# Kernel tuning notes

Measured on AMD Instinct MI355X. Metric: run time of the kernel, lower is better.

The kernel has to match this reference:

```python
import jax, jax.numpy as jnp
import numpy as np

B, CIN, COUT, N, T, K = 16, 32, 64, 1024, 64, 3


def setup_inputs() -> dict:
    key = jax.random.key(0)
    k1, k2, k3 = jax.random.split(key, 3)
    x = jax.random.normal(k1, (B, CIN, N, T), dtype=jnp.float32)
    # scaled laplacian-like support (keep spectral radius ~1 so Chebyshev terms stay bounded)
    adj = jax.random.normal(k2, (N, N), dtype=jnp.float32) / np.sqrt(N).astype(np.float32)
    W = jax.random.normal(k3, (4 * COUT, (CIN + COUT) * K), dtype=jnp.float32) * 0.02
    b = jnp.zeros((4 * COUT,), dtype=jnp.float32)
    return {"x": x, "adj": adj, "W": W, "b": b}


def reference(x, adj, W, b):
    Bn, cin, Nn, Tn = x.shape
    c_out = W.shape[0] // 4
    feat_in = W.shape[1] // K  # = cin + c_out

    # Chebyshev polynomial basis of adj (loop-invariant across time; compute once)
    Ls = [jnp.eye(Nn, dtype=x.dtype), adj]
    for _ in range(2, K):
        Ls.append(2.0 * (adj @ Ls[-1]) - Ls[-2])
    Lap = jnp.stack(Ls, 0)  # [K, N, N]; Ls[k][q, n]

    # Conv1d(kernel=1) weight reshaped to match channel flatten order (c major, k minor)
    Wr = W.reshape(4 * c_out, feat_in, K)  # [4*c_out, F, K]
    bb = b[None, :, None]

    def step(carry, xt):
        h, c = carry
        tem = jnp.concatenate([xt, h], axis=1)  # [B, F, N]
        # einsum('bcn,knq->bckq', x, Lap.T) == einsum('bfn,kqn->bfkq', x, Lap)
        g = jnp.einsum('bfn,kqn->bfkq', tem, Lap)  # [B, F, K, N]
        fea = jnp.einsum('bfkq,ofk->boq', g, Wr) + bb  # [B, 4*c_out, N]
        i, j, f, o = jnp.split(fea, 4, axis=1)
        new_c = c * jax.nn.sigmoid(f) + jax.nn.sigmoid(i) * jnp.tanh(j)
        new_h = jnp.tanh(new_c) * jax.nn.sigmoid(o)
        return (new_h, new_c), new_h

    h0 = jnp.zeros((Bn, c_out, Nn), dtype=x.dtype)
    c0 = jnp.zeros((Bn, c_out, Nn), dtype=x.dtype)
    x_t = jnp.moveaxis(x, -1, 0)  # [T, B, cin, N]
    _, outs = jax.lax.scan(step, (h0, c0), x_t)  # [T, B, c_out, N]
    return jnp.moveaxis(outs, 0, -1)  # [B, c_out, N, T]
```

## Files before the change

kernel.cpp:

```cpp
#include <hip/hip_runtime.h>
#include <stdint.h>


#define Bb   16
#define CIN  32
#define COUT 64
#define Nn   1024
#define Tt   64
#define Ff   96
#define G4   256
#define KJ   288

#define BUFSZ 40960
#define GQPB  624
#define GQLO  19968

typedef unsigned short u16;
typedef short short8 __attribute__((ext_vector_type(8)));
typedef short short4v __attribute__((ext_vector_type(4)));
typedef float f32x4 __attribute__((ext_vector_type(4)));

static __device__ __forceinline__ u16 f2bf(float f) {
    union { float f; uint32_t u; } v; v.f = f;
    uint32_t r = v.u + 0x7FFFu + ((v.u >> 16) & 1u);
    return (u16)(r >> 16);
}
static __device__ __forceinline__ float bf2f(u16 h) {
    union { uint32_t u; float f; } v; v.u = ((uint32_t)h) << 16;
    return v.f;
}
static __device__ __forceinline__ float sigm(float x) { return 1.0f / (1.0f + expf(-x)); }

static __device__ __forceinline__ void gload16(const void* g, void* l) {
    __builtin_amdgcn_global_load_lds(
        (const __attribute__((address_space(1))) void*)g,
        (__attribute__((address_space(3))) void*)l, 16, 0, 0);
}

__global__ void k_fill(float* out, int n, float v) {
    int i = blockIdx.x * 256 + threadIdx.x;
    if (i < n) out[i] = v;
}

__global__ __launch_bounds__(256) void k_adj_split(const float* __restrict__ adj,
                                                   u16* __restrict__ hi, u16* __restrict__ lo) {
    int i = blockIdx.x * 256 + threadIdx.x;
    float v = adj[i];
    u16 h = f2bf(v);
    hi[i] = h; lo[i] = f2bf(v - bf2f(h));
}

__global__ __launch_bounds__(256) void k_adj_t(const float* __restrict__ adj,
                                               u16* __restrict__ th, u16* __restrict__ tl_) {
    __shared__ float tile[64][65];
    int m0 = blockIdx.x * 64, n0 = blockIdx.y * 64;
    int tid = threadIdx.x;
    #pragma unroll
    for (int i = 0; i < 16; i++) {
        int lin = i * 256 + tid;
        int ml = lin >> 6, nl = lin & 63;
        tile[ml][nl] = adj[(size_t)(m0 + ml) * Nn + n0 + nl];
    }
    __syncthreads();
    #pragma unroll
    for (int i = 0; i < 16; i++) {
        int lin = i * 256 + tid;
        int nl = lin >> 6, ml = lin & 63;
        float v = tile[ml][nl];
        u16 h = f2bf(v);
        size_t off = (size_t)(n0 + nl) * Nn + m0 + ml;
        th[off] = h; tl_[off] = f2bf(v - bf2f(h));
    }
}

__global__ __launch_bounds__(256) void k_l2(
    const u16* __restrict__ a_hi, const u16* __restrict__ a_lo,
    const u16* __restrict__ bt_hi, const u16* __restrict__ bt_lo,
    u16* __restrict__ o_hi, u16* __restrict__ o_lo)
{
    __shared__ u16 Ah[64][40], Al[64][40], Bh[64][40], Bl[64][40];
    const int tid = threadIdx.x, lane = tid & 63, w = tid >> 6;
    const int wm = (w >> 1) * 32, wn = (w & 1) * 32;
    const int r0 = blockIdx.x * 64, q0 = blockIdx.y * 64;
    const int srow = tid >> 2, scol = (tid & 3) * 8;
    const u16* arh = a_hi + (size_t)(r0 + srow) * Nn;
    const u16* arl = a_lo + (size_t)(r0 + srow) * Nn;
    const u16* brh = bt_hi + (size_t)(q0 + srow) * Nn;
    const u16* brl = bt_lo + (size_t)(q0 + srow) * Nn;

    f32x4 acc[2][2];
    #pragma unroll
    for (int i = 0; i < 2; i++)
        #pragma unroll
        for (int j = 0; j < 2; j++) acc[i][j] = (f32x4){0.f, 0.f, 0.f, 0.f};

    for (int k0 = 0; k0 < Nn; k0 += 32) {
        __syncthreads();
        *(short8*)&Ah[srow][scol] = *(const short8*)&arh[k0 + scol];
        *(short8*)&Al[srow][scol] = *(const short8*)&arl[k0 + scol];
        *(short8*)&Bh[srow][scol] = *(const short8*)&brh[k0 + scol];
        *(short8*)&Bl[srow][scol] = *(const short8*)&brl[k0 + scol];
        __syncthreads();
        const int kb = (lane >> 4) * 8;
        short8 ah[2], al[2], bh[2], bl[2];
        #pragma unroll
        for (int mi = 0; mi < 2; mi++) {
            int row = wm + mi * 16 + (lane & 15);
            ah[mi] = *(const short8*)&Ah[row][kb];
            al[mi] = *(const short8*)&Al[row][kb];
        }
        #pragma unroll
        for (int ni = 0; ni < 2; ni++) {
            int col = wn + ni * 16 + (lane & 15);
            bh[ni] = *(const short8*)&Bh[col][kb];
            bl[ni] = *(const short8*)&Bl[col][kb];
        }
        #pragma unroll
        for (int mi = 0; mi < 2; mi++)
            #pragma unroll
            for (int ni = 0; ni < 2; ni++) {
                acc[mi][ni] = __builtin_amdgcn_mfma_f32_16x16x32_bf16(ah[mi], bh[ni], acc[mi][ni], 0, 0, 0);
                acc[mi][ni] = __builtin_amdgcn_mfma_f32_16x16x32_bf16(al[mi], bh[ni], acc[mi][ni], 0, 0, 0);
                acc[mi][ni] = __builtin_amdgcn_mfma_f32_16x16x32_bf16(ah[mi], bl[ni], acc[mi][ni], 0, 0, 0);
            }
    }
    #pragma unroll
    for (int mi = 0; mi < 2; mi++)
        #pragma unroll
        for (int ni = 0; ni < 2; ni++)
            #pragma unroll
            for (int j = 0; j < 4; j++) {
                int rr = r0 + wm + mi * 16 + (lane >> 4) * 4 + j;
                int qq = q0 + wn + ni * 16 + (lane & 15);
                float v = 2.f * acc[mi][ni][j] - ((rr == qq) ? 1.f : 0.f);
                size_t off = (size_t)rr * Nn + qq;
                u16 hh = f2bf(v);
                o_hi[off] = hh; o_lo[off] = f2bf(v - bf2f(hh));
            }
}

__global__ __launch_bounds__(256) void k_w_split(const float* __restrict__ W,
                                                 u16* __restrict__ hi, u16* __restrict__ lo) {
    int idx = blockIdx.x * 256 + threadIdx.x;
    int o = idx / KJ, j = idx - o * KJ;
    int k = j / Ff, f = j - k * Ff;
    float v = W[(size_t)o * KJ + f * 3 + k];
    u16 h = f2bf(v);
    hi[idx] = h; lo[idx] = f2bf(v - bf2f(h));
}

__global__ __launch_bounds__(256) void k_x_split(const float* __restrict__ x,
        u16* __restrict__ xf_hi, u16* __restrict__ xf_lo) {
    __shared__ float tile[64][65];
    int n0 = blockIdx.x * 64;
    int bc = blockIdx.y;
    const float* src = x + (size_t)bc * Nn * Tt;
    int tid = threadIdx.x;
    #pragma unroll
    for (int i = 0; i < 16; i++) {
        int lin = i * 256 + tid;
        int nl = lin >> 6, tl = lin & 63;
        tile[nl][tl] = src[(size_t)(n0 + nl) * Tt + tl];
    }
    __syncthreads();
    int b = bc >> 5, ch = bc & 31;
    #pragma unroll
    for (int i = 0; i < 16; i++) {
        int lin = i * 256 + tid;
        int tl = lin >> 6, nl = lin & 63;
        float v = tile[nl][tl];
        u16 h = f2bf(v), l = f2bf(v - bf2f(h));
        size_t off = (((size_t)tl * Bb + b) * CIN + ch) * Nn + n0 + nl;
        xf_hi[off] = h; xf_lo[off] = l;
    }
}

__global__ __launch_bounds__(512, 4) void k_step(
    int t,
    const u16* __restrict__ xsf_hi, const u16* __restrict__ xsf_lo,
    u16* __restrict__ hf_hi, u16* __restrict__ hf_lo,
    const u16* __restrict__ bcat_hi, const u16* __restrict__ bcat_lo,
    const u16* __restrict__ Wh, const u16* __restrict__ Wl,
    const float* __restrict__ bias, float* __restrict__ cbuf,
    float* __restrict__ outbuf)
{
    __shared__ __attribute__((aligned(16))) char lds[81920];
    const int tid = threadIdx.x, lane = tid & 63, w = tid >> 6;
    const int bx = blockIdx.x;
    const int q0g = bx * 32;
    const int bb = blockIdx.y;

    const u16* srcb[5];
    #pragma unroll
    for (int i = 0; i < 5; i++) {
        int u = i * 512 + tid;
        if (u < 1536) {
            int hl = (u >= 768) ? 1 : 0;
            int r = (u - hl * 768) >> 3, c8 = u & 7;
            const u16* p;
            if (r < CIN) p = (hl ? xsf_lo : xsf_hi) + (size_t)((t * Bb + bb) * CIN + r) * Nn;
            else         p = (hl ? hf_lo  : hf_hi ) + (size_t)(bb * COUT + r - CIN) * Nn;
            srcb[i] = p + (c8 ^ (r & 7)) * 8;
        } else {
            int v = u - 1536;
            int hl = v >> 9;
            int r = (v & 511) >> 3, c8 = v & 7;
            int grow = q0g + (r & 31) + ((r >= 32) ? Nn : 0);
            srcb[i] = (hl ? bcat_lo : bcat_hi) + (size_t)grow * Nn + (c8 ^ (r & 7)) * 8;
        }
    }

    const int wr = w >> 2, wc = w & 3;
    f32x4 acc[3];
    #pragma unroll
    for (int i = 0; i < 3; i++) acc[i] = (f32x4){0.f, 0.f, 0.f, 0.f};

    u16 cxh[6], cxl[6];
    #pragma unroll
    for (int i = 0; i < 6; i++) { cxh[i] = 0; cxl[i] = 0; }
    const int capkc = bx >> 1;

    #pragma unroll
    for (int i = 0; i < 5; i++)
        gload16(srcb[i], lds + (i * 512 + tid) * 16);

    for (int kc = 0; kc < 16; kc++) {
        if (kc < 15) {
            char* nb = lds + ((kc + 1) & 1) * BUFSZ;
            const int k0 = (kc + 1) * 64;
            #pragma unroll
            for (int i = 0; i < 5; i++)
                gload16(srcb[i] + k0, nb + (i * 512 + tid) * 16);
            asm volatile("s_waitcnt vmcnt(5)" ::: "memory");
        } else {
            asm volatile("s_waitcnt vmcnt(0)" ::: "memory");
        }
        __builtin_amdgcn_s_barrier();
        const char* bo = lds + (kc & 1) * BUFSZ;
        #pragma unroll
        for (int kk = 0; kk < 2; kk++) {
            const int ksw = kk * 4 + (lane >> 4);
            short8 ah[3], al[3], bh, bl;
            #pragma unroll
            for (int mi = 0; mi < 3; mi++) {
                int r = wr * 48 + mi * 16 + (lane & 15);
                int off = r * 128 + ((ksw ^ (r & 7)) << 4);
                ah[mi] = *(const short8*)(bo + off);
                al[mi] = *(const short8*)(bo + 12288 + off);
            }
            {
                int rb = wc * 16 + (lane & 15);
                int off = 24576 + rb * 128 + ((ksw ^ (rb & 7)) << 4);
                bh = *(const short8*)(bo + off);
                bl = *(const short8*)(bo + 8192 + off);
            }
            #pragma unroll
            for (int mi = 0; mi < 3; mi++) {
                acc[mi] = __builtin_amdgcn_mfma_f32_16x16x32_bf16(ah[mi], bh, acc[mi], 0, 0, 0);
                acc[mi] = __builtin_amdgcn_mfma_f32_16x16x32_bf16(al[mi], bh, acc[mi], 0, 0, 0);
                acc[mi] = __builtin_amdgcn_mfma_f32_16x16x32_bf16(ah[mi], bl, acc[mi], 0, 0, 0);
            }
        }
        if (kc == capkc) {
            int q = lane & 31;
            int jg = (w << 1) | (lane >> 5);
            int lc = ((bx & 1) << 5) | q;
            int u8 = lc >> 3, byoff = (lc & 7) * 2;
            #pragma unroll
            for (int jj = 0; jj < 6; jj++) {
                int j = jg * 6 + jj;
                int off = j * 128 + (((u8) ^ (j & 7)) << 4) + byoff;
                cxh[jj] = *(const u16*)(bo + off);
                cxl[jj] = *(const u16*)(bo + 12288 + off);
            }
            asm volatile("s_waitcnt lgkmcnt(0)" ::: "memory");
            __builtin_amdgcn_sched_barrier(0);
        }
        __builtin_amdgcn_s_barrier();
    }

    {
        int q = lane & 31;
        int jg = (w << 1) | (lane >> 5);
        #pragma unroll
        for (int jj = 0; jj < 6; jj++) {
            int j = jg * 6 + jj;
            *(u16*)(lds + q * GQPB + j * 2) = cxh[jj];
            *(u16*)(lds + GQLO + q * GQPB + j * 2) = cxl[jj];
        }
    }
    #pragma unroll
    for (int mi = 0; mi < 3; mi++) {
        int c = wc * 16 + (lane & 15);
        int g = c >> 5, ql = c & 31;
        int f0 = wr * 48 + mi * 16 + (lane >> 4) * 4;
        int jd = 96 + g * 96 + f0;
        short4v vh, vl;
        #pragma unroll
        for (int j = 0; j < 4; j++) {
            float v = acc[mi][j];
            u16 hh = f2bf(v);
            vh[j] = (short)hh;
            vl[j] = (short)f2bf(v - bf2f(hh));
        }
        *(short4v*)(lds + ql * GQPB + jd * 2) = vh;
        *(short4v*)(lds + GQLO + ql * GQPB + jd * 2) = vl;
    }
    __syncthreads();

    f32x4 a2[2][2];
    #pragma unroll
    for (int i = 0; i < 2; i++)
        #pragma unroll
        for (int j = 0; j < 2; j++) a2[i][j] = (f32x4){0.f, 0.f, 0.f, 0.f};

    const int kb8 = (lane >> 4) * 8;
    #pragma unroll
    for (int c = 0; c < 9; c++) {
        int j0 = c * 32;
        short8 wh[2], wl2[2], gh[2], gl[2];
        #pragma unroll
        for (int mi = 0; mi < 2; mi++) {
            int o = w * 32 + mi * 16 + (lane & 15);
            size_t so = (size_t)o * KJ + j0 + kb8;
            wh[mi]  = *(const short8*)&Wh[so];
            wl2[mi] = *(const short8*)&Wl[so];
        }
        #pragma unroll
        for (int ni = 0; ni < 2; ni++) {
            int q = ni * 16 + (lane & 15);
            int off = q * GQPB + (j0 + kb8) * 2;
            gh[ni] = *(const short8*)(lds + off);
            gl[ni] = *(const short8*)(lds + GQLO + off);
        }
        #pragma unroll
        for (int mi = 0; mi < 2; mi++)
            #pragma unroll
            for (int ni = 0; ni < 2; ni++) {
                a2[mi][ni] = __builtin_amdgcn_mfma_f32_16x16x32_bf16(wh[mi],  gh[ni], a2[mi][ni], 0, 0, 0);
                a2[mi][ni] = __builtin_amdgcn_mfma_f32_16x16x32_bf16(wl2[mi], gh[ni], a2[mi][ni], 0, 0, 0);
                a2[mi][ni] = __builtin_amdgcn_mfma_f32_16x16x32_bf16(wh[mi],  gl[ni], a2[mi][ni], 0, 0, 0);
            }
    }
    __syncthreads();

    {
        float* FEAf = (float*)lds;
        #pragma unroll
        for (int mi = 0; mi < 2; mi++) {
            int o0 = w * 32 + mi * 16 + (lane >> 4) * 4;
            f32x4 bv = *(const f32x4*)&bias[o0];
            #pragma unroll
            for (int ni = 0; ni < 2; ni++) {
                int q = ni * 16 + (lane & 15);
                #pragma unroll
                for (int j = 0; j < 4; j++)
                    FEAf[(o0 + j) * 33 + q] = a2[mi][ni][j] + bv[j];
            }
        }
    }
    __syncthreads();

    {
        const float* FEAf = (const float*)lds;
        int q = tid & 31, qg = q0g + q;
        int co0 = (tid >> 5) * 4;
        #pragma unroll
        for (int ii = 0; ii < 4; ii++) {
            int co = co0 + ii;
            float iv = FEAf[co * 33 + q];
            float jv = FEAf[(co + 64) * 33 + q];
            float fv = FEAf[(co + 128) * 33 + q];
            float ov = FEAf[(co + 192) * 33 + q];
            size_t cof = ((size_t)(bb * COUT + co)) * Nn + qg;
            float cc = cbuf[cof];
            float nc = cc * sigm(fv) + sigm(iv) * tanhf(jv);
            float nh = tanhf(nc) * sigm(ov);
            cbuf[cof] = nc;
            u16 hh = f2bf(nh);
            hf_hi[cof] = hh; hf_lo[cof] = f2bf(nh - bf2f(hh));
            outbuf[((size_t)(t * Bb + bb) * COUT + co) * Nn + qg] = nh;
        }
    }
}

__global__ __launch_bounds__(256) void k_out_t(const float* __restrict__ outbuf,
                                               float* __restrict__ out) {
    __shared__ float tile[64][65];
    int q0 = blockIdx.x * 64;
    int bo = blockIdx.y;
    int b = bo >> 6, o = bo & 63;
    int tid = threadIdx.x;
    #pragma unroll
    for (int i = 0; i < 16; i++) {
        int lin = i * 256 + tid;
        int tl = lin >> 6, ql = lin & 63;
        tile[tl][ql] = outbuf[(((size_t)tl * Bb + b) * COUT + o) * Nn + q0 + ql];
    }
    __syncthreads();
    #pragma unroll
    for (int i = 0; i < 16; i++) {
        int lin = i * 256 + tid;
        int ql = lin >> 6, tl = lin & 63;
        out[((size_t)bo * Nn + q0 + ql) * Tt + tl] = tile[tl][ql];
    }
}

extern "C" void kernel_launch(void* const* d_in, const int* in_sizes, int n_in,
                              void* d_out, int out_size, void* d_ws, size_t ws_size,
                              hipStream_t stream)
{
    const float* x    = (const float*)d_in[0];
    const float* adj  = (const float*)d_in[1];
    const float* W    = (const float*)d_in[2];
    const float* bias = (const float*)d_in[3];
    float* out = (float*)d_out;

    size_t off = 0;
    char* base = (char*)d_ws;
    auto take = [&](size_t bytes) -> void* {
        void* r = base + off;
        off += (bytes + 255) & ~(size_t)255;
        return r;
    };
    u16* bcat_hi = (u16*)take(2ull * 2 * Nn * Nn);
    u16* bcat_lo = (u16*)take(2ull * 2 * Nn * Nn);
    u16* adjT_hi = (u16*)take(2ull * Nn * Nn);
    u16* adjT_lo = (u16*)take(2ull * Nn * Nn);
    u16* xsf_hi  = (u16*)take(2ull * Tt * Bb * CIN * Nn);
    u16* xsf_lo  = (u16*)take(2ull * Tt * Bb * CIN * Nn);
    u16* hf_hi   = (u16*)take(2ull * Bb * COUT * Nn);
    u16* hf_lo   = (u16*)take(2ull * Bb * COUT * Nn);
    float* cbuf  = (float*)take(4ull * Bb * COUT * Nn);
    u16* Wc_hi   = (u16*)take(2ull * G4 * KJ);
    u16* Wc_lo   = (u16*)take(2ull * G4 * KJ);
    float* outbuf = (float*)take(4ull * (size_t)Tt * Bb * COUT * Nn);

    if (off > ws_size) {
        float v = (float)(ws_size >> 20);
        k_fill<<<dim3((out_size + 255) / 256), 256, 0, stream>>>(out, out_size, v);
        return;
    }

    hipMemsetAsync(hf_hi, 0, 2ull * Bb * COUT * Nn, stream);
    hipMemsetAsync(hf_lo, 0, 2ull * Bb * COUT * Nn, stream);
    hipMemsetAsync(cbuf, 0, 4ull * Bb * COUT * Nn, stream);

    k_adj_split<<<dim3((Nn * Nn) / 256), 256, 0, stream>>>(adj, bcat_hi, bcat_lo);
    k_adj_t<<<dim3(16, 16), 256, 0, stream>>>(adj, adjT_hi, adjT_lo);
    k_l2<<<dim3(16, 16), 256, 0, stream>>>(bcat_hi, bcat_lo, adjT_hi, adjT_lo,
                                           bcat_hi + (size_t)Nn * Nn, bcat_lo + (size_t)Nn * Nn);
    k_w_split<<<dim3((G4 * KJ) / 256), 256, 0, stream>>>(W, Wc_hi, Wc_lo);
    k_x_split<<<dim3(Nn / 64, Bb * CIN), 256, 0, stream>>>(x, xsf_hi, xsf_lo);

    for (int t = 0; t < Tt; t++) {
        k_step<<<dim3(32, 16), 512, 0, stream>>>(t,
            xsf_hi, xsf_lo, hf_hi, hf_lo,
            bcat_hi, bcat_lo, Wc_hi, Wc_lo,
            bias, cbuf, outbuf);
    }
    k_out_t<<<dim3(Nn / 64, Bb * COUT), 256, 0, stream>>>(outbuf, out);
}
```

Baseline: 2.565 ms.

## Double k_step tile to 64 nodes with 1024-thread blocks and swizzled grid

```diff
diff --git a/kernel.cpp b/kernel.cpp
--- a/kernel.cpp
+++ b/kernel.cpp
@@ -11,9 +11,12 @@
 #define G4   256
 #define KJ   288
 
-#define BUFSZ 40960
+#define BUFSZ 65536
+#define AOLO  12288
+#define BOHI  24576
+#define BOLO  40960
 #define GQPB  624
-#define GQLO  19968
+#define GQLO  39936
 
 typedef unsigned short u16;
 typedef short short8 __attribute__((ext_vector_type(8)));
@@ -165,17 +168,24 @@
     __syncthreads();
     int b = bc >> 5, ch = bc & 31;
     #pragma unroll
-    for (int i = 0; i < 16; i++) {
-        int lin = i * 256 + tid;
-        int tl = lin >> 6, nl = lin & 63;
-        float v = tile[nl][tl];
-        u16 h = f2bf(v), l = f2bf(v - bf2f(h));
-        size_t off = (((size_t)tl * Bb + b) * CIN + ch) * Nn + n0 + nl;
-        xf_hi[off] = h; xf_lo[off] = l;
-    }
-}
-
-__global__ __launch_bounds__(512, 4) void k_step(
+    for (int i = 0; i < 2; i++) {
+        int item = i * 256 + tid;
+        int tl = item >> 3, oct = item & 7;
+        short8 vh, vl;
+        #pragma unroll
+        for (int m = 0; m < 8; m++) {
+            float v = tile[oct * 8 + m][tl];
+            u16 h = f2bf(v);
+            vh[m] = (short)h;
+            vl[m] = (short)f2bf(v - bf2f(h));
+        }
+        size_t off = (((size_t)tl * Bb + b) * CIN + ch) * Nn + n0 + oct * 8;
+        *(short8*)&xf_hi[off] = vh;
+        *(short8*)&xf_lo[off] = vl;
+    }
+}
+
+__global__ __launch_bounds__(1024, 4) void k_step(
     int t,
     const u16* __restrict__ xsf_hi, const u16* __restrict__ xsf_lo,
     u16* __restrict__ hf_hi, u16* __restrict__ hf_lo,
@@ -184,16 +194,18 @@
     const float* __restrict__ bias, float* __restrict__ cbuf,
     float* __restrict__ outbuf)
 {
-    __shared__ __attribute__((aligned(16))) char lds[81920];
+    __shared__ __attribute__((aligned(16))) char lds[131072];
     const int tid = threadIdx.x, lane = tid & 63, w = tid >> 6;
-    const int bx = blockIdx.x;
-    const int q0g = bx * 32;
-    const int bb = blockIdx.y;
-
-    const u16* srcb[5];
-    #pragma unroll
-    for (int i = 0; i < 5; i++) {
-        int u = i * 512 + tid;
+    const int bid = blockIdx.x;
+    const int swz = (bid & 7) * 32 + (bid >> 3);
+    const int qt = swz >> 4;
+    const int bb = swz & 15;
+    const int q0g = qt * 64;
+
+    const u16* srcb[4];
+    #pragma unroll
+    for (int i = 0; i < 4; i++) {
+        int u = i * 1024 + tid;
         if (u < 1536) {
             int hl = (u >= 768) ? 1 : 0;
             int r = (u - hl * 768) >> 3, c8 = u & 7;
@@ -201,16 +213,18 @@
             if (r < CIN) p = (hl ? xsf_lo : xsf_hi) + (size_t)((t * Bb + bb) * CIN + r) * Nn;
             else         p = (hl ? hf_lo  : hf_hi ) + (size_t)(bb * COUT + r - CIN) * Nn;
             srcb[i] = p + (c8 ^ (r & 7)) * 8;
+        } else if (u < 3584) {
+            int v = u - 1536;
+            int hl = v >> 10;
+            int r = (v & 1023) >> 3, c8 = v & 7;
+            int grow = q0g + (r & 63) + ((r >= 64) ? Nn : 0);
+            srcb[i] = (hl ? bcat_lo : bcat_hi) + (size_t)grow * Nn + (c8 ^ (r & 7)) * 8;
         } else {
-            int v = u - 1536;
-            int hl = v >> 9;
-            int r = (v & 511) >> 3, c8 = v & 7;
-            int grow = q0g + (r & 31) + ((r >= 32) ? Nn : 0);
-            srcb[i] = (hl ? bcat_lo : bcat_hi) + (size_t)grow * Nn + (c8 ^ (r & 7)) * 8;
-        }
-    }
-
-    const int wr = w >> 2, wc = w & 3;
+            srcb[i] = bcat_hi + (u & 1023) * 8;
+        }
+    }
+
+    const int wr = w >> 3, wc = w & 7;
     f32x4 acc[3];
     #pragma unroll
     for (int i = 0; i < 3; i++) acc[i] = (f32x4){0.f, 0.f, 0.f, 0.f};
@@ -218,20 +232,19 @@
     u16 cxh[6], cxl[6];
     #pragma unroll
     for (int i = 0; i < 6; i++) { cxh[i] = 0; cxl[i] = 0; }
-    const int capkc = bx >> 1;
-
-    #pragma unroll
-    for (int i = 0; i < 5; i++)
-        gload16(srcb[i], lds + (i * 512 + tid) * 16);
+
+    #pragma unroll
+    for (int i = 0; i < 4; i++)
+        gload16(srcb[i], lds + (i * 1024 + tid) * 16);
 
     for (int kc = 0; kc < 16; kc++) {
         if (kc < 15) {
             char* nb = lds + ((kc + 1) & 1) * BUFSZ;
             const int k0 = (kc + 1) * 64;
             #pragma unroll
-            for (int i = 0; i < 5; i++)
-                gload16(srcb[i] + k0, nb + (i * 512 + tid) * 16);
-            asm volatile("s_waitcnt vmcnt(5)" ::: "memory");
+            for (int i = 0; i < 4; i++)
+                gload16(srcb[i] + k0, nb + (i * 1024 + tid) * 16);
+            asm volatile("s_waitcnt vmcnt(4)" ::: "memory");
         } else {
             asm volatile("s_waitcnt vmcnt(0)" ::: "memory");
         }
@@ -246,13 +259,13 @@
                 int r = wr * 48 + mi * 16 + (lane & 15);
                 int off = r * 128 + ((ksw ^ (r & 7)) << 4);
                 ah[mi] = *(const short8*)(bo + off);
-                al[mi] = *(const short8*)(bo + 12288 + off);
+                al[mi] = *(const short8*)(bo + AOLO + off);
             }
             {
                 int rb = wc * 16 + (lane & 15);
-                int off = 24576 + rb * 128 + ((ksw ^ (rb & 7)) << 4);
-                bh = *(const short8*)(bo + off);
-                bl = *(const short8*)(bo + 8192 + off);
+                int off = rb * 128 + ((ksw ^ (rb & 7)) << 4);
+                bh = *(const short8*)(bo + BOHI + off);
+                bl = *(const short8*)(bo + BOLO + off);
             }
             #pragma unroll
             for (int mi = 0; mi < 3; mi++) {
@@ -261,17 +274,13 @@
                 acc[mi] = __builtin_amdgcn_mfma_f32_16x16x32_bf16(ah[mi], bl, acc[mi], 0, 0, 0);
             }
         }
-        if (kc == capkc) {
-            int q = lane & 31;
-            int jg = (w << 1) | (lane >> 5);
-            int lc = ((bx & 1) << 5) | q;
-            int u8 = lc >> 3, byoff = (lc & 7) * 2;
+        if (kc == qt) {
             #pragma unroll
             for (int jj = 0; jj < 6; jj++) {
-                int j = jg * 6 + jj;
-                int off = j * 128 + (((u8) ^ (j & 7)) << 4) + byoff;
+                int j = w * 6 + jj;
+                int off = j * 128 + ((((lane >> 3)) ^ (j & 7)) << 4) + (lane & 7) * 2;
                 cxh[jj] = *(const u16*)(bo + off);
-                cxl[jj] = *(const u16*)(bo + 12288 + off);
+                cxl[jj] = *(const u16*)(bo + AOLO + off);
             }
             asm volatile("s_waitcnt lgkmcnt(0)" ::: "memory");
             __builtin_amdgcn_sched_barrier(0);
@@ -280,19 +289,17 @@
     }
 
     {
-        int q = lane & 31;
-        int jg = (w << 1) | (lane >> 5);
         #pragma unroll
         for (int jj = 0; jj < 6; jj++) {
-            int j = jg * 6 + jj;
-            *(u16*)(lds + q * GQPB + j * 2) = cxh[jj];
-            *(u16*)(lds + GQLO + q * GQPB + j * 2) = cxl[jj];
+            int j = w * 6 + jj;
+            *(u16*)(lds + lane * GQPB + j * 2) = cxh[jj];
+            *(u16*)(lds + GQLO + lane * GQPB + j * 2) = cxl[jj];
         }
     }
     #pragma unroll
     for (int mi = 0; mi < 3; mi++) {
         int c = wc * 16 + (lane & 15);
-        int g = c >> 5, ql = c & 31;
+        int g = c >> 6, ql = c & 63;
         int f0 = wr * 48 + mi * 16 + (lane >> 4) * 4;
         int jd = 96 + g * 96 + f0;
         short4v vh, vl;
@@ -314,6 +321,7 @@
         #pragma unroll
         for (int j = 0; j < 2; j++) a2[i][j] = (f32x4){0.f, 0.f, 0.f, 0.f};
 
+    const int wo = w >> 1, wq = w & 1;
     const int kb8 = (lane >> 4) * 8;
     #pragma unroll
     for (int c = 0; c < 9; c++) {
@@ -321,14 +329,14 @@
         short8 wh[2], wl2[2], gh[2], gl[2];
         #pragma unroll
         for (int mi = 0; mi < 2; mi++) {
-            int o = w * 32 + mi * 16 + (lane & 15);
+            int o = wo * 32 + mi * 16 + (lane & 15);
             size_t so = (size_t)o * KJ + j0 + kb8;
             wh[mi]  = *(const short8*)&Wh[so];
             wl2[mi] = *(const short8*)&Wl[so];
         }
         #pragma unroll
         for (int ni = 0; ni < 2; ni++) {
-            int q = ni * 16 + (lane & 15);
+            int q = wq * 32 + ni * 16 + (lane & 15);
             int off = q * GQPB + (j0 + kb8) * 2;
             gh[ni] = *(const short8*)(lds + off);
             gl[ni] = *(const short8*)(lds + GQLO + off);
@@ -348,14 +356,14 @@
         float* FEAf = (float*)lds;
         #pragma unroll
         for (int mi = 0; mi < 2; mi++) {
-            int o0 = w * 32 + mi * 16 + (lane >> 4) * 4;
+            int o0 = wo * 32 + mi * 16 + (lane >> 4) * 4;
             f32x4 bv = *(const f32x4*)&bias[o0];
             #pragma unroll
             for (int ni = 0; ni < 2; ni++) {
-                int q = ni * 16 + (lane & 15);
+                int q = wq * 32 + ni * 16 + (lane & 15);
                 #pragma unroll
                 for (int j = 0; j < 4; j++)
-                    FEAf[(o0 + j) * 33 + q] = a2[mi][ni][j] + bv[j];
+                    FEAf[(o0 + j) * 65 + q] = a2[mi][ni][j] + bv[j];
             }
         }
     }
@@ -363,15 +371,15 @@
 
     {
         const float* FEAf = (const float*)lds;
-        int q = tid & 31, qg = q0g + q;
-        int co0 = (tid >> 5) * 4;
+        int q = tid & 63, qg = q0g + q;
+        int co0 = (tid >> 6) * 4;
         #pragma unroll
         for (int ii = 0; ii < 4; ii++) {
             int co = co0 + ii;
-            float iv = FEAf[co * 33 + q];
-            float jv = FEAf[(co + 64) * 33 + q];
-            float fv = FEAf[(co + 128) * 33 + q];
-            float ov = FEAf[(co + 192) * 33 + q];
+            float iv = FEAf[co * 65 + q];
+            float jv = FEAf[(co + 64) * 65 + q];
+            float fv = FEAf[(co + 128) * 65 + q];
+            float ov = FEAf[(co + 192) * 65 + q];
             size_t cof = ((size_t)(bb * COUT + co)) * Nn + qg;
             float cc = cbuf[cof];
             float nc = cc * sigm(fv) + sigm(iv) * tanhf(jv);
@@ -454,7 +462,7 @@
     k_x_split<<<dim3(Nn / 64, Bb * CIN), 256, 0, stream>>>(x, xsf_hi, xsf_lo);
 
     for (int t = 0; t < Tt; t++) {
-        k_step<<<dim3(32, 16), 512, 0, stream>>>(t,
+        k_step<<<dim3(256), 1024, 0, stream>>>(t,
             xsf_hi, xsf_lo, hf_hi, hf_lo,
             bcat_hi, bcat_lo, Wc_hi, Wc_lo,
             bias, cbuf, outbuf);
```

New measurement: 2.783 ms. 8.5% more time.

## Split graph GEMM K across wave groups, widen per-wave tile, vectorize x split stores

Applied to the files above, without the earlier changes.

```diff
diff --git a/kernel.cpp b/kernel.cpp
--- a/kernel.cpp
+++ b/kernel.cpp
@@ -14,6 +14,7 @@
 #define BUFSZ 40960
 #define GQPB  624
 #define GQLO  19968
+#define SCP   100
 
 typedef unsigned short u16;
 typedef short short8 __attribute__((ext_vector_type(8)));
@@ -165,13 +166,20 @@
     __syncthreads();
     int b = bc >> 5, ch = bc & 31;
     #pragma unroll
-    for (int i = 0; i < 16; i++) {
-        int lin = i * 256 + tid;
-        int tl = lin >> 6, nl = lin & 63;
-        float v = tile[nl][tl];
-        u16 h = f2bf(v), l = f2bf(v - bf2f(h));
-        size_t off = (((size_t)tl * Bb + b) * CIN + ch) * Nn + n0 + nl;
-        xf_hi[off] = h; xf_lo[off] = l;
+    for (int i = 0; i < 2; i++) {
+        int item = i * 256 + tid;
+        int tl = item >> 3, oct = item & 7;
+        short8 vh, vl;
+        #pragma unroll
+        for (int m = 0; m < 8; m++) {
+            float v = tile[oct * 8 + m][tl];
+            u16 h = f2bf(v);
+            vh[m] = (short)h;
+            vl[m] = (short)f2bf(v - bf2f(h));
+        }
+        size_t off = (((size_t)tl * Bb + b) * CIN + ch) * Nn + n0 + oct * 8;
+        *(short8*)&xf_hi[off] = vh;
+        *(short8*)&xf_lo[off] = vl;
     }
 }
 
@@ -210,10 +218,16 @@
         }
     }
 
-    const int wr = w >> 2, wc = w & 3;
-    f32x4 acc[3];
-    #pragma unroll
-    for (int i = 0; i < 3; i++) acc[i] = (f32x4){0.f, 0.f, 0.f, 0.f};
+    const int kg = w >> 2;
+    const int wsub = w & 3;
+    const int wr = wsub >> 1, wc = wsub & 1;
+    const int ksw = kg * 4 + (lane >> 4);
+
+    f32x4 acc[3][2];
+    #pragma unroll
+    for (int i = 0; i < 3; i++)
+        #pragma unroll
+        for (int j = 0; j < 2; j++) acc[i][j] = (f32x4){0.f, 0.f, 0.f, 0.f};
 
     u16 cxh[6], cxl[6];
     #pragma unroll
@@ -237,10 +251,8 @@
         }
         __builtin_amdgcn_s_barrier();
         const char* bo = lds + (kc & 1) * BUFSZ;
-        #pragma unroll
-        for (int kk = 0; kk < 2; kk++) {
-            const int ksw = kk * 4 + (lane >> 4);
-            short8 ah[3], al[3], bh, bl;
+        {
+            short8 ah[3], al[3], bh[2], bl[2];
             #pragma unroll
             for (int mi = 0; mi < 3; mi++) {
                 int r = wr * 48 + mi * 16 + (lane & 15);
@@ -248,18 +260,23 @@
                 ah[mi] = *(const short8*)(bo + off);
                 al[mi] = *(const short8*)(bo + 12288 + off);
             }
-            {
-                int rb = wc * 16 + (lane & 15);
+            #pragma unroll
+            for (int ni = 0; ni < 2; ni++) {
+                int rb = wc * 32 + ni * 16 + (lane & 15);
                 int off = 24576 + rb * 128 + ((ksw ^ (rb & 7)) << 4);
-                bh = *(const short8*)(bo + off);
-                bl = *(const short8*)(bo + 8192 + off);
-            }
-            #pragma unroll
-            for (int mi = 0; mi < 3; mi++) {
-                acc[mi] = __builtin_amdgcn_mfma_f32_16x16x32_bf16(ah[mi], bh, acc[mi], 0, 0, 0);
-                acc[mi] = __builtin_amdgcn_mfma_f32_16x16x32_bf16(al[mi], bh, acc[mi], 0, 0, 0);
-                acc[mi] = __builtin_amdgcn_mfma_f32_16x16x32_bf16(ah[mi], bl, acc[mi], 0, 0, 0);
-            }
+                bh[ni] = *(const short8*)(bo + off);
+                bl[ni] = *(const short8*)(bo + 8192 + off);
+            }
+            __builtin_amdgcn_s_setprio(1);
+            #pragma unroll
+            for (int mi = 0; mi < 3; mi++)
+                #pragma unroll
+                for (int ni = 0; ni < 2; ni++) {
+                    acc[mi][ni] = __builtin_amdgcn_mfma_f32_16x16x32_bf16(ah[mi], bh[ni], acc[mi][ni], 0, 0, 0);
+                    acc[mi][ni] = __builtin_amdgcn_mfma_f32_16x16x32_bf16(al[mi], bh[ni], acc[mi][ni], 0, 0, 0);
+                    acc[mi][ni] = __builtin_amdgcn_mfma_f32_16x16x32_bf16(ah[mi], bl[ni], acc[mi][ni], 0, 0, 0);
+                }
+            __builtin_amdgcn_s_setprio(0);
         }
         if (kc == capkc) {
             int q = lane & 31;
@@ -280,6 +297,31 @@
     }
 
     {
+        float* scratch = (float*)(lds + BUFSZ);
+        if (kg == 0) {
+            #pragma unroll
+            for (int mi = 0; mi < 3; mi++)
+                #pragma unroll
+                for (int ni = 0; ni < 2; ni++) {
+                    int c = wc * 32 + ni * 16 + (lane & 15);
+                    int r0 = wr * 48 + mi * 16 + (lane >> 4) * 4;
+                    *(f32x4*)&scratch[c * SCP + r0] = acc[mi][ni];
+                }
+        }
+        __syncthreads();
+        if (kg == 1) {
+            #pragma unroll
+            for (int mi = 0; mi < 3; mi++)
+                #pragma unroll
+                for (int ni = 0; ni < 2; ni++) {
+                    int c = wc * 32 + ni * 16 + (lane & 15);
+                    int r0 = wr * 48 + mi * 16 + (lane >> 4) * 4;
+                    acc[mi][ni] += *(const f32x4*)&scratch[c * SCP + r0];
+                }
+        }
+    }
+
+    {
         int q = lane & 31;
         int jg = (w << 1) | (lane >> 5);
         #pragma unroll
@@ -289,22 +331,26 @@
             *(u16*)(lds + GQLO + q * GQPB + j * 2) = cxl[jj];
         }
     }
-    #pragma unroll
-    for (int mi = 0; mi < 3; mi++) {
-        int c = wc * 16 + (lane & 15);
-        int g = c >> 5, ql = c & 31;
-        int f0 = wr * 48 + mi * 16 + (lane >> 4) * 4;
-        int jd = 96 + g * 96 + f0;
-        short4v vh, vl;
-        #pragma unroll
-        for (int j = 0; j < 4; j++) {
-            float v = acc[mi][j];
-            u16 hh = f2bf(v);
-            vh[j] = (short)hh;
-            vl[j] = (short)f2bf(v - bf2f(hh));
-        }
-        *(short4v*)(lds + ql * GQPB + jd * 2) = vh;
-        *(short4v*)(lds + GQLO + ql * GQPB + jd * 2) = vl;
+    if (kg == 1) {
+        #pragma unroll
+        for (int mi = 0; mi < 3; mi++)
+            #pragma unroll
+            for (int ni = 0; ni < 2; ni++) {
+                int c = wc * 32 + ni * 16 + (lane & 15);
+                int g = c >> 5, ql = c & 31;
+                int f0 = wr * 48 + mi * 16 + (lane >> 4) * 4;
+                int jd = 96 + g * 96 + f0;
+                short4v vh, vl;
+                #pragma unroll
+                for (int j = 0; j < 4; j++) {
+                    float v = acc[mi][ni][j];
+                    u16 hh = f2bf(v);
+                    vh[j] = (short)hh;
+                    vl[j] = (short)f2bf(v - bf2f(hh));
+                }
+                *(short4v*)(lds + ql * GQPB + jd * 2) = vh;
+                *(short4v*)(lds + GQLO + ql * GQPB + jd * 2) = vl;
+            }
     }
     __syncthreads();
 
```

Result: faster. 2.514 ms (-2.0%).

## Halve k-chunk size, shrink LDS, ping-pong hidden state, vectorize x split

Applied to the files above, without the earlier changes.

```diff
diff --git a/kernel.cpp b/kernel.cpp
--- a/kernel.cpp
+++ b/kernel.cpp
@@ -11,9 +11,14 @@
 #define G4   256
 #define KJ   288
 
-#define BUFSZ 40960
+#define BUFSZ 20480
+#define AHI   0
+#define ALO   6144
+#define BHI   12288
+#define BLO   16384
 #define GQPB  624
 #define GQLO  19968
+#define NCHUNK 32
 
 typedef unsigned short u16;
 typedef short short8 __attribute__((ext_vector_type(8)));
@@ -165,52 +170,68 @@
     __syncthreads();
     int b = bc >> 5, ch = bc & 31;
     #pragma unroll
-    for (int i = 0; i < 16; i++) {
-        int lin = i * 256 + tid;
-        int tl = lin >> 6, nl = lin & 63;
-        float v = tile[nl][tl];
-        u16 h = f2bf(v), l = f2bf(v - bf2f(h));
-        size_t off = (((size_t)tl * Bb + b) * CIN + ch) * Nn + n0 + nl;
-        xf_hi[off] = h; xf_lo[off] = l;
-    }
-}
-
-__global__ __launch_bounds__(512, 4) void k_step(
+    for (int i = 0; i < 2; i++) {
+        int item = i * 256 + tid;
+        int tl = item >> 3, oct = item & 7;
+        short8 vh, vl;
+        #pragma unroll
+        for (int m = 0; m < 8; m++) {
+            float v = tile[oct * 8 + m][tl];
+            u16 h = f2bf(v);
+            vh[m] = (short)h;
+            vl[m] = (short)f2bf(v - bf2f(h));
+        }
+        size_t off = (((size_t)tl * Bb + b) * CIN + ch) * Nn + n0 + oct * 8;
+        *(short8*)&xf_hi[off] = vh;
+        *(short8*)&xf_lo[off] = vl;
+    }
+}
+
+__global__ __launch_bounds__(512, 8) void k_step(
     int t,
     const u16* __restrict__ xsf_hi, const u16* __restrict__ xsf_lo,
-    u16* __restrict__ hf_hi, u16* __restrict__ hf_lo,
+    const u16* __restrict__ hin_hi, const u16* __restrict__ hin_lo,
+    u16* __restrict__ hout_hi, u16* __restrict__ hout_lo,
     const u16* __restrict__ bcat_hi, const u16* __restrict__ bcat_lo,
     const u16* __restrict__ Wh, const u16* __restrict__ Wl,
     const float* __restrict__ bias, float* __restrict__ cbuf,
     float* __restrict__ outbuf)
 {
-    __shared__ __attribute__((aligned(16))) char lds[81920];
+    __shared__ __attribute__((aligned(16))) char lds[40960];
     const int tid = threadIdx.x, lane = tid & 63, w = tid >> 6;
     const int bx = blockIdx.x;
     const int q0g = bx * 32;
     const int bb = blockIdx.y;
 
-    const u16* srcb[5];
-    #pragma unroll
-    for (int i = 0; i < 5; i++) {
-        int u = i * 512 + tid;
-        if (u < 1536) {
-            int hl = (u >= 768) ? 1 : 0;
-            int r = (u - hl * 768) >> 3, c8 = u & 7;
+    const u16* srcb[3];
+    #pragma unroll
+    for (int i = 0; i < 3; i++) {
+        int u = i * 512 + ((i == 2) ? (tid & 255) : tid);
+        if (u < 768) {
+            int hl = (u >= 384) ? 1 : 0;
+            int ua = u - hl * 384;
+            int R = ua >> 3, sp = ua & 7;
+            int s = sp ^ (R & 7);
+            int r = 2 * R + (s >> 2), c4 = s & 3;
             const u16* p;
             if (r < CIN) p = (hl ? xsf_lo : xsf_hi) + (size_t)((t * Bb + bb) * CIN + r) * Nn;
-            else         p = (hl ? hf_lo  : hf_hi ) + (size_t)(bb * COUT + r - CIN) * Nn;
-            srcb[i] = p + (c8 ^ (r & 7)) * 8;
+            else         p = (hl ? hin_lo : hin_hi) + (size_t)(bb * COUT + r - CIN) * Nn;
+            srcb[i] = p + c4 * 8;
         } else {
-            int v = u - 1536;
-            int hl = v >> 9;
-            int r = (v & 511) >> 3, c8 = v & 7;
-            int grow = q0g + (r & 31) + ((r >= 32) ? Nn : 0);
-            srcb[i] = (hl ? bcat_lo : bcat_hi) + (size_t)grow * Nn + (c8 ^ (r & 7)) * 8;
+            int hl = (u >= 1024) ? 1 : 0;
+            int ub = u - 768 - hl * 256;
+            int R = ub >> 3, sp = ub & 7;
+            int s = sp ^ (R & 7);
+            int rloc = 2 * R + (s >> 2), c4 = s & 3;
+            int grow = q0g + (rloc & 31) + ((rloc >= 32) ? Nn : 0);
+            srcb[i] = (hl ? bcat_lo : bcat_hi) + (size_t)grow * Nn + c4 * 8;
         }
     }
 
     const int wr = w >> 2, wc = w & 3;
+    const int ksw = lane >> 4;
+    const int capkc = bx;
+
     f32x4 acc[3];
     #pragma unroll
     for (int i = 0; i < 3; i++) acc[i] = (f32x4){0.f, 0.f, 0.f, 0.f};
@@ -218,60 +239,64 @@
     u16 cxh[6], cxl[6];
     #pragma unroll
     for (int i = 0; i < 6; i++) { cxh[i] = 0; cxl[i] = 0; }
-    const int capkc = bx >> 1;
-
-    #pragma unroll
-    for (int i = 0; i < 5; i++)
-        gload16(srcb[i], lds + (i * 512 + tid) * 16);
-
-    for (int kc = 0; kc < 16; kc++) {
-        if (kc < 15) {
+
+    gload16(srcb[0], lds + (size_t)tid * 16);
+    gload16(srcb[1], lds + (size_t)(512 + tid) * 16);
+    if (tid < 256) gload16(srcb[2], lds + (size_t)(1024 + tid) * 16);
+
+    for (int kc = 0; kc < NCHUNK; kc++) {
+        if (kc < NCHUNK - 1) {
             char* nb = lds + ((kc + 1) & 1) * BUFSZ;
-            const int k0 = (kc + 1) * 64;
-            #pragma unroll
-            for (int i = 0; i < 5; i++)
-                gload16(srcb[i] + k0, nb + (i * 512 + tid) * 16);
-            asm volatile("s_waitcnt vmcnt(5)" ::: "memory");
+            const int k0 = (kc + 1) * 32;
+            gload16(srcb[0] + k0, nb + (size_t)tid * 16);
+            gload16(srcb[1] + k0, nb + (size_t)(512 + tid) * 16);
+            if (tid < 256) gload16(srcb[2] + k0, nb + (size_t)(1024 + tid) * 16);
+            if (w < 4) { asm volatile("s_waitcnt vmcnt(3)" ::: "memory"); }
+            else       { asm volatile("s_waitcnt vmcnt(2)" ::: "memory"); }
         } else {
             asm volatile("s_waitcnt vmcnt(0)" ::: "memory");
         }
         __builtin_amdgcn_s_barrier();
         const char* bo = lds + (kc & 1) * BUFSZ;
-        #pragma unroll
-        for (int kk = 0; kk < 2; kk++) {
-            const int ksw = kk * 4 + (lane >> 4);
+        {
             short8 ah[3], al[3], bh, bl;
             #pragma unroll
             for (int mi = 0; mi < 3; mi++) {
                 int r = wr * 48 + mi * 16 + (lane & 15);
-                int off = r * 128 + ((ksw ^ (r & 7)) << 4);
-                ah[mi] = *(const short8*)(bo + off);
-                al[mi] = *(const short8*)(bo + 12288 + off);
+                int R = r >> 1;
+                int sp = (4 * (r & 1) + ksw) ^ (R & 7);
+                int off = R * 128 + sp * 16;
+                ah[mi] = *(const short8*)(bo + AHI + off);
+                al[mi] = *(const short8*)(bo + ALO + off);
             }
             {
                 int rb = wc * 16 + (lane & 15);
-                int off = 24576 + rb * 128 + ((ksw ^ (rb & 7)) << 4);
-                bh = *(const short8*)(bo + off);
-                bl = *(const short8*)(bo + 8192 + off);
-            }
+                int R = rb >> 1;
+                int sp = (4 * (rb & 1) + ksw) ^ (R & 7);
+                int off = R * 128 + sp * 16;
+                bh = *(const short8*)(bo + BHI + off);
+                bl = *(const short8*)(bo + BLO + off);
+            }
+            __builtin_amdgcn_s_setprio(1);
             #pragma unroll
             for (int mi = 0; mi < 3; mi++) {
                 acc[mi] = __builtin_amdgcn_mfma_f32_16x16x32_bf16(ah[mi], bh, acc[mi], 0, 0, 0);
                 acc[mi] = __builtin_amdgcn_mfma_f32_16x16x32_bf16(al[mi], bh, acc[mi], 0, 0, 0);
                 acc[mi] = __builtin_amdgcn_mfma_f32_16x16x32_bf16(ah[mi], bl, acc[mi], 0, 0, 0);
             }
+            __builtin_amdgcn_s_setprio(0);
         }
         if (kc == capkc) {
             int q = lane & 31;
             int jg = (w << 1) | (lane >> 5);
-            int lc = ((bx & 1) << 5) | q;
-            int u8 = lc >> 3, byoff = (lc & 7) * 2;
             #pragma unroll
             for (int jj = 0; jj < 6; jj++) {
                 int j = jg * 6 + jj;
-                int off = j * 128 + (((u8) ^ (j & 7)) << 4) + byoff;
-                cxh[jj] = *(const u16*)(bo + off);
-                cxl[jj] = *(const u16*)(bo + 12288 + off);
+                int R = j >> 1;
+                int sp = (4 * (j & 1) + (q >> 3)) ^ (R & 7);
+                int off = R * 128 + sp * 16 + (q & 7) * 2;
+                cxh[jj] = *(const u16*)(bo + AHI + off);
+                cxl[jj] = *(const u16*)(bo + ALO + off);
             }
             asm volatile("s_waitcnt lgkmcnt(0)" ::: "memory");
             __builtin_amdgcn_sched_barrier(0);
@@ -378,7 +403,7 @@
             float nh = tanhf(nc) * sigm(ov);
             cbuf[cof] = nc;
             u16 hh = f2bf(nh);
-            hf_hi[cof] = hh; hf_lo[cof] = f2bf(nh - bf2f(hh));
+            hout_hi[cof] = hh; hout_lo[cof] = f2bf(nh - bf2f(hh));
             outbuf[((size_t)(t * Bb + bb) * COUT + co) * Nn + qg] = nh;
         }
     }
@@ -429,8 +454,10 @@
     u16* adjT_lo = (u16*)take(2ull * Nn * Nn);
     u16* xsf_hi  = (u16*)take(2ull * Tt * Bb * CIN * Nn);
     u16* xsf_lo  = (u16*)take(2ull * Tt * Bb * CIN * Nn);
-    u16* hf_hi   = (u16*)take(2ull * Bb * COUT * Nn);
-    u16* hf_lo   = (u16*)take(2ull * Bb * COUT * Nn);
+    u16* hfA_hi  = (u16*)take(2ull * Bb * COUT * Nn);
+    u16* hfA_lo  = (u16*)take(2ull * Bb * COUT * Nn);
+    u16* hfB_hi  = (u16*)take(2ull * Bb * COUT * Nn);
+    u16* hfB_lo  = (u16*)take(2ull * Bb * COUT * Nn);
     float* cbuf  = (float*)take(4ull * Bb * COUT * Nn);
     u16* Wc_hi   = (u16*)take(2ull * G4 * KJ);
     u16* Wc_lo   = (u16*)take(2ull * G4 * KJ);
@@ -442,8 +469,8 @@
         return;
     }
 
-    hipMemsetAsync(hf_hi, 0, 2ull * Bb * COUT * Nn, stream);
-    hipMemsetAsync(hf_lo, 0, 2ull * Bb * COUT * Nn, stream);
+    hipMemsetAsync(hfA_hi, 0, 2ull * Bb * COUT * Nn, stream);
+    hipMemsetAsync(hfA_lo, 0, 2ull * Bb * COUT * Nn, stream);
     hipMemsetAsync(cbuf, 0, 4ull * Bb * COUT * Nn, stream);
 
     k_adj_split<<<dim3((Nn * Nn) / 256), 256, 0, stream>>>(adj, bcat_hi, bcat_lo);
@@ -454,8 +481,12 @@
     k_x_split<<<dim3(Nn / 64, Bb * CIN), 256, 0, stream>>>(x, xsf_hi, xsf_lo);
 
     for (int t = 0; t < Tt; t++) {
+        const u16* hi_in  = (t & 1) ? hfB_hi : hfA_hi;
+        const u16* lo_in  = (t & 1) ? hfB_lo : hfA_lo;
+        u16* hi_out = (t & 1) ? hfA_hi : hfB_hi;
+        u16* lo_out = (t & 1) ? hfA_lo : hfB_lo;
         k_step<<<dim3(32, 16), 512, 0, stream>>>(t,
-            xsf_hi, xsf_lo, hf_hi, hf_lo,
+            xsf_hi, xsf_lo, hi_in, lo_in, hi_out, lo_out,
             bcat_hi, bcat_lo, Wc_hi, Wc_lo,
             bias, cbuf, outbuf);
     }
```

New measurement: 3.019 ms. +17.7%, slower.
